# Kernel tuning notes

Hardware: AMD Instinct MI355X
Metric: run time of the kernel (lower is better)

The kernel has to match this reference:

```python
import jax, jax.numpy as jnp
import numpy as np

V, D, H, L, T_MAX = 50257, 1024, 16, 12, 256
HS = D // H
B, T = 8, 256


def setup_inputs() -> dict:
    key = jax.random.key(0)
    ks = jax.random.split(key, 24)
    s = 0.02
    inp = {
        'idx': jax.random.randint(ks[0], (B, T), 0, V),
        'targets': jax.random.randint(ks[1], (B, T), 0, V),
        'tok_emb': jax.random.normal(ks[2], (V, D), jnp.float32) * s,
        'pos_emb': jax.random.normal(ks[3], (T_MAX, D), jnp.float32) * s,
        'Wq': jax.random.normal(ks[4], (L, H, D, HS), jnp.float32) / np.sqrt(D),
        'Wk': jax.random.normal(ks[5], (L, H, D, HS), jnp.float32) / np.sqrt(D),
        'Wv': jax.random.normal(ks[6], (L, H, D, HS), jnp.float32) / np.sqrt(D),
        'ln1_g': jnp.ones((L, D), jnp.float32),
        'ln1_b': jnp.zeros((L, D), jnp.float32),
        'ln2_g': jnp.ones((L, D), jnp.float32),
        'ln2_b': jnp.zeros((L, D), jnp.float32),
        'fc1_w': jax.random.normal(ks[7], (L, D, 4 * D), jnp.float32) / np.sqrt(D),
        'fc1_b': jnp.zeros((L, 4 * D), jnp.float32),
        'fc2_w': jax.random.normal(ks[8], (L, 4 * D, D), jnp.float32) / np.sqrt(4 * D),
        'fc2_b': jnp.zeros((L, D), jnp.float32),
        'lnf_g': jnp.ones((D,), jnp.float32),
        'lnf_b': jnp.zeros((D,), jnp.float32),
        'lm_w': jax.random.normal(ks[9], (D, V), jnp.float32) / np.sqrt(D),
        'lm_b': jnp.zeros((V,), jnp.float32),
    }
    return inp


def _layernorm(x, g, b, eps=1e-5):
    mu = jnp.mean(x, axis=-1, keepdims=True)
    var = jnp.var(x, axis=-1, keepdims=True)
    return (x - mu) * jax.lax.rsqrt(var + eps) * g + b


def reference(idx, targets, tok_emb, pos_emb, Wq, Wk, Wv, ln1_g, ln1_b, ln2_g, ln2_b,
              fc1_w, fc1_b, fc2_w, fc2_b, lnf_g, lnf_b, lm_w, lm_b):
    Bc, Tc = idx.shape
    x = tok_emb[idx] + pos_emb[:Tc]  # [B,T,D]
    causal = jnp.tril(jnp.ones((Tc, Tc), bool))
    scale = 1.0 / np.sqrt(HS)
    for l in range(L):
        h = _layernorm(x, ln1_g[l], ln1_b[l])
        q = jnp.einsum('btd,hds->bhts', h, Wq[l])
        k = jnp.einsum('btd,hds->bhts', h, Wk[l])
        v = jnp.einsum('btd,hds->bhts', h, Wv[l])
        scores = jnp.einsum('bhts,bhus->bhtu', q, k) * scale
        scores = jnp.where(causal, scores, -jnp.inf)
        attn = jax.nn.softmax(scores, axis=-1)
        o = jnp.einsum('bhtu,bhus->bhts', attn, v)  # [B,H,T,hs]
        o = o.transpose(0, 2, 1, 3).reshape(Bc, Tc, D)  # concat heads
        x = x + o  # no output projection in original
        h = _layernorm(x, ln2_g[l], ln2_b[l])
        ff = jax.nn.relu(h @ fc1_w[l] + fc1_b[l]) @ fc2_w[l] + fc2_b[l]
        x = x + ff
    x = _layernorm(x, lnf_g, lnf_b)
    logits = x @ lm_w + lm_b  # [B,T,V]
    logp = jax.nn.log_softmax(logits, axis=-1)
    nll = -jnp.take_along_axis(logp, targets[..., None], axis=-1)[..., 0]
    loss = jnp.mean(nll)
    return logits, loss
```

## Files before the change

kernel.cpp:

```cpp
#include <hip/hip_runtime.h>

#define T_SEQ 256
#define DMODEL 1024
#define NHEAD 16
#define HSZ 64
#define NLAYER 12
#define VOCAB 50257
#define NPAD 50304
#define FF 4096
#define MROWS 2048

using short8 = __attribute__((ext_vector_type(8))) short;
using f32x4  = __attribute__((ext_vector_type(4))) float;

__device__ __forceinline__ float bf2f(unsigned short u) {
    unsigned int x = ((unsigned int)u) << 16;
    return __builtin_bit_cast(float, x);
}
__device__ __forceinline__ unsigned short f2bf(float f) {
    unsigned int u = __builtin_bit_cast(unsigned int, f);
    unsigned int r = (u + 0x7fffu + ((u >> 16) & 1u)) >> 16;
    return (unsigned short)r;
}
__device__ __forceinline__ void async_copy16(const void* g, void* l) {
    __builtin_amdgcn_global_load_lds(
        (const __attribute__((address_space(1))) unsigned int*)g,
        (__attribute__((address_space(3))) unsigned int*)l, 16, 0, 0);
}

__global__ __launch_bounds__(256) void embed_kernel(
    const int* __restrict__ idx, const float* __restrict__ tok,
    const float* __restrict__ pos, float* __restrict__ x)
{
    int row = blockIdx.x, tid = threadIdx.x;
    int t = row & (T_SEQ - 1);
    int token = idx[row];
    float4 a = ((const float4*)(tok + (size_t)token * DMODEL))[tid];
    float4 p = ((const float4*)(pos + (size_t)t * DMODEL))[tid];
    float4 o;
    o.x = a.x + p.x; o.y = a.y + p.y; o.z = a.z + p.z; o.w = a.w + p.w;
    ((float4*)(x + (size_t)row * DMODEL))[tid] = o;
}

__global__ __launch_bounds__(256) void ln_kernel(
    const float* __restrict__ x, const float* __restrict__ g,
    const float* __restrict__ b, unsigned short* __restrict__ out)
{
    int row = blockIdx.x, tid = threadIdx.x;
    float4 v = ((const float4*)(x + (size_t)row * DMODEL))[tid];
    float s  = v.x + v.y + v.z + v.w;
    float ss = v.x * v.x + v.y * v.y + v.z * v.z + v.w * v.w;
    for (int o = 32; o > 0; o >>= 1) {
        s  += __shfl_down(s, o);
        ss += __shfl_down(ss, o);
    }
    __shared__ float ps[4], pss[4];
    int wave = tid >> 6, lane = tid & 63;
    if (lane == 0) { ps[wave] = s; pss[wave] = ss; }
    __syncthreads();
    float st  = ps[0] + ps[1] + ps[2] + ps[3];
    float sst = pss[0] + pss[1] + pss[2] + pss[3];
    float mu  = st * (1.0f / DMODEL);
    float var = sst * (1.0f / DMODEL) - mu * mu;
    float rstd = rsqrtf(var + 1e-5f);
    float4 gv = ((const float4*)g)[tid];
    float4 bv = ((const float4*)b)[tid];
    ushort4 o4;
    o4.x = f2bf((v.x - mu) * rstd * gv.x + bv.x);
    o4.y = f2bf((v.y - mu) * rstd * gv.y + bv.y);
    o4.z = f2bf((v.z - mu) * rstd * gv.z + bv.z);
    o4.w = f2bf((v.w - mu) * rstd * gv.w + bv.w);
    ((ushort4*)out)[(size_t)row * (DMODEL / 4) + tid] = o4;
}

__global__ __launch_bounds__(256) void wtranspose_kernel(
    const float* __restrict__ in, unsigned short* __restrict__ out,
    int R, int C, int Cout, long in_l, long out_l)
{
    int lyr = blockIdx.z;
    in  += (size_t)lyr * in_l;
    out += (size_t)lyr * out_l;
    __shared__ float tile[32][33];
    int tx = threadIdx.x & 31, ty = threadIdx.x >> 5;
    int c0 = blockIdx.x * 32, r0 = blockIdx.y * 32;
    #pragma unroll
    for (int i = 0; i < 4; i++) {
        int r = r0 + ty + i * 8, c = c0 + tx;
        tile[ty + i * 8][tx] = (c < C) ? in[(size_t)r * C + c] : 0.f;
    }
    __syncthreads();
    #pragma unroll
    for (int i = 0; i < 4; i++) {
        int c = c0 + ty + i * 8, r = r0 + tx;
        if (c < Cout) out[(size_t)c * R + r] = f2bf(tile[tx][ty + i * 8]);
    }
}

__global__ __launch_bounds__(256) void qkvpack_kernel(
    const float* __restrict__ Wq, const float* __restrict__ Wk,
    const float* __restrict__ Wv, unsigned short* __restrict__ out,
    long w_l, long out_l)
{
    int z = blockIdx.z;
    int lyr = z / 48, r48 = z % 48;
    int seg = r48 >> 4, hh = r48 & 15;
    const float* W = (seg == 0 ? Wq : seg == 1 ? Wk : Wv)
                     + (size_t)lyr * w_l + (size_t)hh * DMODEL * HSZ;
    unsigned short* o = out + (size_t)lyr * out_l
                      + (size_t)(seg * 1024 + hh * 64) * DMODEL;
    __shared__ float tile[32][33];
    int tx = threadIdx.x & 31, ty = threadIdx.x >> 5;
    int d0 = blockIdx.x * 32, s0 = blockIdx.y * 32;
    #pragma unroll
    for (int i = 0; i < 4; i++)
        tile[ty + i * 8][tx] = W[(size_t)(d0 + ty + i * 8) * HSZ + s0 + tx];
    __syncthreads();
    #pragma unroll
    for (int i = 0; i < 4; i++)
        o[(size_t)(s0 + ty + i * 8) * DMODEL + d0 + tx] = f2bf(tile[tx][ty + i * 8]);
}

template<int MF, bool QKV, bool RELU, bool RES, bool CBF16>
__device__ __forceinline__ void gemm_core(
    const unsigned short* __restrict__ A, int lda,
    const unsigned short* __restrict__ Bt, int ldb,
    const float* __restrict__ bias,
    void* __restrict__ Cv, int ldc,
    const float* __restrict__ res, int ldr,
    int N, int K,
    unsigned short* __restrict__ vtout)
{
    constexpr int BM = MF * 32;
    __shared__ __align__(16) char As[BM * 128];
    __shared__ __align__(16) char Bs[128 * 128];
    int tid = threadIdx.x;
    int wave = tid >> 6, lane = tid & 63;
    int wr = wave >> 1, wc = wave & 1;
    int m0 = blockIdx.x * BM, n0 = blockIdx.y * 128;

    f32x4 acc[MF][4];
    #pragma unroll
    for (int m = 0; m < MF; m++)
        #pragma unroll
        for (int n = 0; n < 4; n++)
            acc[m][n] = (f32x4){0.f, 0.f, 0.f, 0.f};

    int ksw = (((lane & 7) ^ (lane >> 3)) << 4);
    int KT = K >> 6;
    for (int kt = 0; kt < KT; kt++) {
        int k0 = kt << 6;
        __syncthreads();
        #pragma unroll
        for (int j = 0; j < MF; j++) {
            int row = (wave * MF + j) * 8 + (lane >> 3);
            const char* src = (const char*)A + ((size_t)(m0 + row) * lda + k0) * 2 + ksw;
            async_copy16(src, As + (wave * MF + j) * 1024);
        }
        #pragma unroll
        for (int j = 0; j < 4; j++) {
            int nrow = (wave * 4 + j) * 8 + (lane >> 3);
            const char* src = (const char*)Bt + ((size_t)(n0 + nrow) * ldb + k0) * 2 + ksw;
            async_copy16(src, Bs + (wave * 4 + j) * 1024);
        }
        __syncthreads();
        #pragma unroll
        for (int ks = 0; ks < 2; ks++) {
            int kb = ks * 64 + ((lane >> 4) << 4);
            short8 a[MF], b[4];
            #pragma unroll
            for (int m = 0; m < MF; m++) {
                int r = wr * (MF * 16) + m * 16 + (lane & 15);
                a[m] = *(const short8*)(const void*)(As + r * 128 + (kb ^ ((r & 7) << 4)));
            }
            #pragma unroll
            for (int n = 0; n < 4; n++) {
                int c = wc * 64 + n * 16 + (lane & 15);
                b[n] = *(const short8*)(const void*)(Bs + c * 128 + (kb ^ ((c & 7) << 4)));
            }
            #pragma unroll
            for (int m = 0; m < MF; m++)
                #pragma unroll
                for (int n = 0; n < 4; n++)
                    acc[m][n] = __builtin_amdgcn_mfma_f32_16x16x32_bf16(a[m], b[n], acc[m][n], 0, 0, 0);
        }
    }
    #pragma unroll
    for (int m = 0; m < MF; m++) {
        int rowb = m0 + wr * (MF * 16) + m * 16 + ((lane >> 4) << 2);
        #pragma unroll
        for (int n = 0; n < 4; n++) {
            int col = n0 + wc * 64 + n * 16 + (lane & 15);
            if (col < N) {
                float bi = bias ? bias[col] : 0.f;
                #pragma unroll
                for (int r2 = 0; r2 < 4; r2++) {
                    float v = acc[m][n][r2] + bi;
                    if (RELU) v = fmaxf(v, 0.f);
                    int row = rowb + r2;
                    if (RES) v += res[(size_t)row * ldr + col];
                    if (QKV && col >= 2048) {
                        int hh = (col - 2048) >> 6, sdim = (col - 2048) & 63;
                        int bb = row >> 8, tt = row & 255;
                        vtout[((((size_t)bb * NHEAD + hh) * HSZ + sdim) * T_SEQ) + tt] = f2bf(v);
                    } else if (CBF16) {
                        ((unsigned short*)Cv)[(size_t)row * ldc + col] = f2bf(v);
                    } else {
                        ((float*)Cv)[(size_t)row * ldc + col] = v;
                    }
                }
            }
        }
    }
}

__global__ __launch_bounds__(256) void gemm_qkv(
    const unsigned short* __restrict__ A, const unsigned short* __restrict__ Bt,
    unsigned short* __restrict__ C, unsigned short* __restrict__ vtout)
{
    gemm_core<4, true, false, false, true>(
        A, DMODEL, Bt, DMODEL, nullptr, C, 3072, nullptr, 0, 3072, DMODEL, vtout);
}

__global__ __launch_bounds__(256) void gemm_fc1(
    const unsigned short* __restrict__ A, const unsigned short* __restrict__ Bt,
    const float* __restrict__ bias, unsigned short* __restrict__ C)
{
    gemm_core<4, false, true, false, true>(
        A, DMODEL, Bt, DMODEL, bias, C, FF, nullptr, 0, FF, DMODEL, nullptr);
}

__global__ __launch_bounds__(256) void gemm_fc2(
    const unsigned short* __restrict__ A, const unsigned short* __restrict__ Bt,
    float* __restrict__ part)
{
    int z = blockIdx.z;
    gemm_core<2, false, false, false, false>(
        A + z * 2048, FF, Bt + z * 2048, FF, nullptr,
        part + (size_t)z * MROWS * DMODEL, DMODEL, nullptr, 0,
        DMODEL, 2048, nullptr);
}

__global__ __launch_bounds__(256) void fc2_merge_kernel(
    const float* __restrict__ part, const float* __restrict__ bias,
    float* __restrict__ x)
{
    int row = blockIdx.x, tid = threadIdx.x;
    size_t o = (size_t)row * DMODEL / 4 + tid;
    float4 p0 = ((const float4*)part)[o];
    float4 p1 = ((const float4*)part)[o + MROWS * DMODEL / 4];
    float4 bv = ((const float4*)bias)[tid];
    float4 xv = ((float4*)x)[o];
    xv.x += p0.x + p1.x + bv.x;
    xv.y += p0.y + p1.y + bv.y;
    xv.z += p0.z + p1.z + bv.z;
    xv.w += p0.w + p1.w + bv.w;
    ((float4*)x)[o] = xv;
}

__global__ __launch_bounds__(256) void gemm_lm(
    const unsigned short* __restrict__ A, const unsigned short* __restrict__ Bt,
    const float* __restrict__ bias, float* __restrict__ C)
{
    gemm_core<4, false, false, false, false>(
        A, DMODEL, Bt, DMODEL, bias, C, VOCAB, nullptr, 0, VOCAB, DMODEL, nullptr);
}

__global__ __launch_bounds__(256) void attn_fused_kernel(
    const unsigned short* __restrict__ qkv, const unsigned short* __restrict__ vt,
    float* __restrict__ x)
{
    int qt = blockIdx.x, hh = blockIdx.y, b = blockIdx.z;
    int tid = threadIdx.x;
    int wave = tid >> 6, lane = tid & 63;
    int g = lane >> 4, q = lane & 15;

    __shared__ __align__(16) char Kb[2][8192];
    __shared__ __align__(16) char Vb[2][8192];
    __shared__ __align__(16) char Plds[4][2048];

    int qrow = b * T_SEQ + qt * 64 + wave * 16 + q;
    const char* qp = (const char*)qkv + ((size_t)qrow * 3072 + hh * HSZ) * 2;
    short8 qreg[2];
    qreg[0] = *(const short8*)(const void*)(qp + (g << 4));
    qreg[1] = *(const short8*)(const void*)(qp + 64 + (g << 4));

    char* Pw = Plds[wave];

    f32x4 oacc[4];
    #pragma unroll
    for (int f = 0; f < 4; f++) oacc[f] = (f32x4){0.f, 0.f, 0.f, 0.f};
    float m_run = -1e30f, l_run = 0.f;

    int srow = wave * 8 + (lane >> 3);
    int sbyte = ((lane & 7) << 4) ^ ((srow & 7) << 4);

    auto stage = [&](int kt, int bi) {
        #pragma unroll
        for (int c = 0; c < 2; c++) {
            int row = c * 32 + srow;
            const char* src = (const char*)qkv +
                ((size_t)(b * T_SEQ + kt * 64 + row) * 3072 + 1024 + hh * HSZ) * 2 + sbyte;
            async_copy16(src, Kb[bi] + c * 4096 + wave * 1024);
        }
        #pragma unroll
        for (int c = 0; c < 2; c++) {
            int row = c * 32 + srow;
            const char* src = (const char*)vt +
                (((size_t)(b * NHEAD + hh) * HSZ + row) * T_SEQ + kt * 64) * 2 + sbyte;
            async_copy16(src, Vb[bi] + c * 4096 + wave * 1024);
        }
    };

    stage(0, 0);
    for (int kt = 0; kt <= qt; kt++) {
        int bi = kt & 1;
        __syncthreads();
        if (kt < qt) stage(kt + 1, bi ^ 1);

        f32x4 sacc[4];
        #pragma unroll
        for (int f = 0; f < 4; f++) sacc[f] = (f32x4){0.f, 0.f, 0.f, 0.f};
        #pragma unroll
        for (int ks = 0; ks < 2; ks++) {
            int kb = ks * 64 + (g << 4);
            #pragma unroll
            for (int f = 0; f < 4; f++) {
                int u = f * 16 + q;
                short8 kf = *(const short8*)(const void*)(Kb[bi] + u * 128 + (kb ^ ((u & 7) << 4)));
                sacc[f] = __builtin_amdgcn_mfma_f32_16x16x32_bf16(kf, qreg[ks], sacc[f], 0, 0, 0);
            }
        }
        float sv[4][4];
        #pragma unroll
        for (int f = 0; f < 4; f++)
            #pragma unroll
            for (int r = 0; r < 4; r++) {
                float v = sacc[f][r] * 0.125f;
                if (kt == qt) {
                    int u_loc = f * 16 + g * 4 + r;
                    if (u_loc > wave * 16 + q) v = -1e30f;
                }
                sv[f][r] = v;
            }
        float pm = -1e30f;
        #pragma unroll
        for (int f = 0; f < 4; f++)
            #pragma unroll
            for (int r = 0; r < 4; r++) pm = fmaxf(pm, sv[f][r]);
        pm = fmaxf(pm, __shfl_xor(pm, 16));
        pm = fmaxf(pm, __shfl_xor(pm, 32));
        float mnew = fmaxf(m_run, pm);
        float corr = __expf(m_run - mnew);
        float p[4][4];
        float ls = 0.f;
        #pragma unroll
        for (int f = 0; f < 4; f++)
            #pragma unroll
            for (int r = 0; r < 4; r++) {
                p[f][r] = __expf(sv[f][r] - mnew);
                ls += p[f][r];
            }
        ls += __shfl_xor(ls, 16);
        ls += __shfl_xor(ls, 32);
        l_run = l_run * corr + ls;
        m_run = mnew;
        #pragma unroll
        for (int r = 0; r < 4; r++) {
            float cr = __shfl(corr, (lane & 48) | (g * 4 + r));
            #pragma unroll
            for (int f = 0; f < 4; f++) oacc[f][r] *= cr;
        }
        #pragma unroll
        for (int f = 0; f < 4; f++)
            #pragma unroll
            for (int rp = 0; rp < 2; rp++) {
                int ue = f * 16 + g * 4 + rp * 2;
                unsigned int pk = (unsigned int)f2bf(p[f][rp * 2])
                                | ((unsigned int)f2bf(p[f][rp * 2 + 1]) << 16);
                *(unsigned int*)(void*)(Pw + q * 128 + ((ue * 2) ^ ((q & 7) << 4))) = pk;
            }
        #pragma unroll
        for (int ks = 0; ks < 2; ks++) {
            int kb = ks * 64 + (g << 4);
            short8 pa = *(const short8*)(const void*)(Pw + q * 128 + (kb ^ ((q & 7) << 4)));
            #pragma unroll
            for (int f = 0; f < 4; f++) {
                int s = f * 16 + q;
                short8 vf = *(const short8*)(const void*)(Vb[bi] + s * 128 + (kb ^ ((s & 7) << 4)));
                oacc[f] = __builtin_amdgcn_mfma_f32_16x16x32_bf16(pa, vf, oacc[f], 0, 0, 0);
            }
        }
    }
    float inv = 1.0f / l_run;
    #pragma unroll
    for (int r = 0; r < 4; r++) {
        float ir = __shfl(inv, (lane & 48) | (g * 4 + r));
        int row_g = b * T_SEQ + qt * 64 + wave * 16 + g * 4 + r;
        #pragma unroll
        for (int f = 0; f < 4; f++) {
            size_t xi = (size_t)row_g * DMODEL + hh * HSZ + f * 16 + q;
            x[xi] += oacc[f][r] * ir;
        }
    }
}

__global__ __launch_bounds__(256) void loss1_kernel(
    const float* __restrict__ logits, const int* __restrict__ targets,
    float* __restrict__ nll)
{
    int r = blockIdx.x, tid = threadIdx.x;
    const float* row = logits + (size_t)r * VOCAB;
    const float4* row4 = (const float4*)row;
    float m = -3.4e38f, s = 0.f;
    for (int v = tid; v < VOCAB / 4; v += 256) {
        float4 x4 = row4[v];
        float lm = fmaxf(fmaxf(x4.x, x4.y), fmaxf(x4.z, x4.w));
        float nm = fmaxf(m, lm);
        s = s * __expf(m - nm) + __expf(x4.x - nm) + __expf(x4.y - nm)
          + __expf(x4.z - nm) + __expf(x4.w - nm);
        m = nm;
    }
    if (tid == 0) {
        float xv = row[VOCAB - 1];
        float nm = fmaxf(m, xv);
        s = s * __expf(m - nm) + __expf(xv - nm);
        m = nm;
    }
    __shared__ float ms[256], ssh[256];
    ms[tid] = m; ssh[tid] = s;
    __syncthreads();
    for (int o = 128; o > 0; o >>= 1) {
        if (tid < o) {
            float m1 = ms[tid], s1 = ssh[tid];
            float m2 = ms[tid + o], s2 = ssh[tid + o];
            float nm = fmaxf(m1, m2);
            ssh[tid] = s1 * __expf(m1 - nm) + s2 * __expf(m2 - nm);
            ms[tid] = nm;
        }
        __syncthreads();
    }
    if (tid == 0) nll[r] = logf(ssh[0]) + ms[0] - row[targets[r]];
}

__global__ __launch_bounds__(256) void loss2_kernel(
    const float* __restrict__ nll, float* __restrict__ out)
{
    int tid = threadIdx.x;
    float s = 0.f;
    for (int i = tid; i < MROWS; i += 256) s += nll[i];
    __shared__ float red[256];
    red[tid] = s;
    __syncthreads();
    for (int o = 128; o > 0; o >>= 1) {
        if (tid < o) red[tid] += red[tid + o];
        __syncthreads();
    }
    if (tid == 0) out[0] = red[0] * (1.0f / MROWS);
}

extern "C" void kernel_launch(void* const* d_in, const int* in_sizes, int n_in,
                              void* d_out, int out_size, void* d_ws, size_t ws_size,
                              hipStream_t stream)
{
    const int*   idx  = (const int*)d_in[0];
    const int*   tgt  = (const int*)d_in[1];
    const float* tok  = (const float*)d_in[2];
    const float* pos  = (const float*)d_in[3];
    const float* Wq   = (const float*)d_in[4];
    const float* Wk   = (const float*)d_in[5];
    const float* Wv   = (const float*)d_in[6];
    const float* ln1g = (const float*)d_in[7];
    const float* ln1b = (const float*)d_in[8];
    const float* ln2g = (const float*)d_in[9];
    const float* ln2b = (const float*)d_in[10];
    const float* fc1w = (const float*)d_in[11];
    const float* fc1b = (const float*)d_in[12];
    const float* fc2w = (const float*)d_in[13];
    const float* fc2b = (const float*)d_in[14];
    const float* lnfg = (const float*)d_in[15];
    const float* lnfb = (const float*)d_in[16];
    const float* lmw  = (const float*)d_in[17];
    const float* lmb  = (const float*)d_in[18];

    char* ws = (char*)d_ws;
    float*          x    = (float*)(ws + 0);
    unsigned short* h    = (unsigned short*)(ws + 8388608);
    unsigned short* qkv  = (unsigned short*)(ws + 12582912);
    unsigned short* vt   = (unsigned short*)(ws + 25165824);
    unsigned short* mid  = (unsigned short*)(ws + 29360128);
    float*          nll  = (float*)(ws + 46137344);
    float*          fc2p = (float*)(ws + 46145536);
    unsigned short* lmwt = (unsigned short*)(ws + 62922752);
    const size_t UP_NEED = 442769408ull;
    bool upfront = (ws_size >= UP_NEED);
    unsigned short* qkvt = (unsigned short*)(ws + 165945344);
    unsigned short* fc1t, * fc2t;
    long qkvt_l, fc1t_l, fc2t_l;
    if (upfront) {
        fc1t = (unsigned short*)(ws + 241442816);
        fc2t = (unsigned short*)(ws + 342106112);
        qkvt_l = 3072 * 1024; fc1t_l = (long)FF * 1024; fc2t_l = (long)1024 * FF;
    } else {
        fc1t = (unsigned short*)(ws + 172236800);
        fc2t = (unsigned short*)(ws + 180625408);
        qkvt_l = 0; fc1t_l = 0; fc2t_l = 0;
    }
    float* logits = (float*)d_out;
    float* lossp  = logits + (size_t)MROWS * VOCAB;

    const long WQKV_L = (long)NHEAD * DMODEL * HSZ;
    if (upfront) {
        qkvpack_kernel<<<dim3(32, 2, 48 * NLAYER), 256, 0, stream>>>(
            Wq, Wk, Wv, qkvt, WQKV_L, qkvt_l);
        wtranspose_kernel<<<dim3(128, 32, NLAYER), 256, 0, stream>>>(
            fc1w, fc1t, DMODEL, FF, FF, (long)DMODEL * FF, fc1t_l);
        wtranspose_kernel<<<dim3(32, 128, NLAYER), 256, 0, stream>>>(
            fc2w, fc2t, FF, DMODEL, DMODEL, (long)FF * DMODEL, fc2t_l);
    }
    wtranspose_kernel<<<dim3(1572, 32, 1), 256, 0, stream>>>(
        lmw, lmwt, DMODEL, VOCAB, NPAD, 0, 0);

    embed_kernel<<<MROWS, 256, 0, stream>>>(idx, tok, pos, x);

    for (int l = 0; l < NLAYER; l++) {
        unsigned short* qkvt_p = qkvt + (size_t)l * qkvt_l;
        unsigned short* fc1t_p = fc1t + (size_t)l * fc1t_l;
        unsigned short* fc2t_p = fc2t + (size_t)l * fc2t_l;
        if (!upfront) {
            qkvpack_kernel<<<dim3(32, 2, 48), 256, 0, stream>>>(
                Wq + (size_t)l * WQKV_L, Wk + (size_t)l * WQKV_L,
                Wv + (size_t)l * WQKV_L, qkvt, WQKV_L, 0);
            wtranspose_kernel<<<dim3(128, 32, 1), 256, 0, stream>>>(
                fc1w + (size_t)l * DMODEL * FF, fc1t, DMODEL, FF, FF, 0, 0);
            wtranspose_kernel<<<dim3(32, 128, 1), 256, 0, stream>>>(
                fc2w + (size_t)l * FF * DMODEL, fc2t, FF, DMODEL, DMODEL, 0, 0);
        }
        ln_kernel<<<MROWS, 256, 0, stream>>>(x, ln1g + l * DMODEL, ln1b + l * DMODEL, h);
        gemm_qkv<<<dim3(16, 24), 256, 0, stream>>>(h, qkvt_p, qkv, vt);
        attn_fused_kernel<<<dim3(4, NHEAD, 8), 256, 0, stream>>>(qkv, vt, x);
        ln_kernel<<<MROWS, 256, 0, stream>>>(x, ln2g + l * DMODEL, ln2b + l * DMODEL, h);
        gemm_fc1<<<dim3(16, 32), 256, 0, stream>>>(h, fc1t_p, fc1b + (size_t)l * FF, mid);
        gemm_fc2<<<dim3(32, 8, 2), 256, 0, stream>>>(mid, fc2t_p, fc2p);
        fc2_merge_kernel<<<MROWS, 256, 0, stream>>>(fc2p, fc2b + (size_t)l * DMODEL, x);
    }

    ln_kernel<<<MROWS, 256, 0, stream>>>(x, lnfg, lnfb, h);
    gemm_lm<<<dim3(16, 393), 256, 0, stream>>>(h, lmwt, lmb, logits);

    loss1_kernel<<<MROWS, 256, 0, stream>>>(logits, tgt, nll);
    loss2_kernel<<<1, 256, 0, stream>>>(nll, lossp);
}
```

Baseline: 2.223 ms.

## Double-buffer GEMM LDS tiles and fuse layernorm into embed and fc2 merge

The shared GEMM core now keeps two LDS buffers and issues the async global-to-LDS loads for the next K tile before computing on the current one, so only one barrier per iteration remains. LDS use per block doubles, which may lower occupancy. The embedding and fc2-merge kernels now also compute the following layernorm (ln1 of the next layer or the final one), removing 13 separate layernorm launches and their re-read of the residual stream.

```diff
diff --git a/kernel.cpp b/kernel.cpp
--- a/kernel.cpp
+++ b/kernel.cpp
@@ -28,26 +28,10 @@
         (__attribute__((address_space(3))) unsigned int*)l, 16, 0, 0);
 }
 
-__global__ __launch_bounds__(256) void embed_kernel(
-    const int* __restrict__ idx, const float* __restrict__ tok,
-    const float* __restrict__ pos, float* __restrict__ x)
-{
-    int row = blockIdx.x, tid = threadIdx.x;
-    int t = row & (T_SEQ - 1);
-    int token = idx[row];
-    float4 a = ((const float4*)(tok + (size_t)token * DMODEL))[tid];
-    float4 p = ((const float4*)(pos + (size_t)t * DMODEL))[tid];
-    float4 o;
-    o.x = a.x + p.x; o.y = a.y + p.y; o.z = a.z + p.z; o.w = a.w + p.w;
-    ((float4*)(x + (size_t)row * DMODEL))[tid] = o;
-}
-
-__global__ __launch_bounds__(256) void ln_kernel(
-    const float* __restrict__ x, const float* __restrict__ g,
-    const float* __restrict__ b, unsigned short* __restrict__ out)
-{
-    int row = blockIdx.x, tid = threadIdx.x;
-    float4 v = ((const float4*)(x + (size_t)row * DMODEL))[tid];
+__device__ __forceinline__ void ln_tail(
+    float4 v, const float* __restrict__ g, const float* __restrict__ b,
+    int row, int tid, unsigned short* __restrict__ out)
+{
     float s  = v.x + v.y + v.z + v.w;
     float ss = v.x * v.x + v.y * v.y + v.z * v.z + v.w * v.w;
     for (int o = 32; o > 0; o >>= 1) {
@@ -73,6 +57,51 @@
     ((ushort4*)out)[(size_t)row * (DMODEL / 4) + tid] = o4;
 }
 
+__global__ __launch_bounds__(256) void embed_ln_kernel(
+    const int* __restrict__ idx, const float* __restrict__ tok,
+    const float* __restrict__ pos, const float* __restrict__ g,
+    const float* __restrict__ b, float* __restrict__ x,
+    unsigned short* __restrict__ h)
+{
+    int row = blockIdx.x, tid = threadIdx.x;
+    int t = row & (T_SEQ - 1);
+    int token = idx[row];
+    float4 a = ((const float4*)(tok + (size_t)token * DMODEL))[tid];
+    float4 p = ((const float4*)(pos + (size_t)t * DMODEL))[tid];
+    float4 v;
+    v.x = a.x + p.x; v.y = a.y + p.y; v.z = a.z + p.z; v.w = a.w + p.w;
+    ((float4*)(x + (size_t)row * DMODEL))[tid] = v;
+    ln_tail(v, g, b, row, tid, h);
+}
+
+__global__ __launch_bounds__(256) void ln_kernel(
+    const float* __restrict__ x, const float* __restrict__ g,
+    const float* __restrict__ b, unsigned short* __restrict__ out)
+{
+    int row = blockIdx.x, tid = threadIdx.x;
+    float4 v = ((const float4*)(x + (size_t)row * DMODEL))[tid];
+    ln_tail(v, g, b, row, tid, out);
+}
+
+__global__ __launch_bounds__(256) void fc2_merge_ln_kernel(
+    const float* __restrict__ part, const float* __restrict__ bias,
+    const float* __restrict__ g, const float* __restrict__ b,
+    float* __restrict__ x, unsigned short* __restrict__ h)
+{
+    int row = blockIdx.x, tid = threadIdx.x;
+    size_t o = (size_t)row * (DMODEL / 4) + tid;
+    float4 p0 = ((const float4*)part)[o];
+    float4 p1 = ((const float4*)part)[o + MROWS * (DMODEL / 4)];
+    float4 bv = ((const float4*)bias)[tid];
+    float4 v = ((float4*)x)[o];
+    v.x += p0.x + p1.x + bv.x;
+    v.y += p0.y + p1.y + bv.y;
+    v.z += p0.z + p1.z + bv.z;
+    v.w += p0.w + p1.w + bv.w;
+    ((float4*)x)[o] = v;
+    ln_tail(v, g, b, row, tid, h);
+}
+
 __global__ __launch_bounds__(256) void wtranspose_kernel(
     const float* __restrict__ in, unsigned short* __restrict__ out,
     int R, int C, int Cout, long in_l, long out_l)
@@ -131,8 +160,8 @@
     unsigned short* __restrict__ vtout)
 {
     constexpr int BM = MF * 32;
-    __shared__ __align__(16) char As[BM * 128];
-    __shared__ __align__(16) char Bs[128 * 128];
+    __shared__ __align__(16) char As[2][BM * 128];
+    __shared__ __align__(16) char Bs[2][128 * 128];
     int tid = threadIdx.x;
     int wave = tid >> 6, lane = tid & 63;
     int wr = wave >> 1, wc = wave & 1;
@@ -147,22 +176,28 @@
 
     int ksw = (((lane & 7) ^ (lane >> 3)) << 4);
     int KT = K >> 6;
-    for (int kt = 0; kt < KT; kt++) {
+
+    auto stage = [&](int kt, int bi) {
         int k0 = kt << 6;
-        __syncthreads();
         #pragma unroll
         for (int j = 0; j < MF; j++) {
             int row = (wave * MF + j) * 8 + (lane >> 3);
             const char* src = (const char*)A + ((size_t)(m0 + row) * lda + k0) * 2 + ksw;
-            async_copy16(src, As + (wave * MF + j) * 1024);
+            async_copy16(src, As[bi] + (wave * MF + j) * 1024);
         }
         #pragma unroll
         for (int j = 0; j < 4; j++) {
             int nrow = (wave * 4 + j) * 8 + (lane >> 3);
             const char* src = (const char*)Bt + ((size_t)(n0 + nrow) * ldb + k0) * 2 + ksw;
-            async_copy16(src, Bs + (wave * 4 + j) * 1024);
-        }
-        __syncthreads();
+            async_copy16(src, Bs[bi] + (wave * 4 + j) * 1024);
+        }
+    };
+
+    stage(0, 0);
+    __syncthreads();
+    int cur = 0;
+    for (int kt = 0; kt < KT; kt++) {
+        if (kt + 1 < KT) stage(kt + 1, cur ^ 1);
         #pragma unroll
         for (int ks = 0; ks < 2; ks++) {
             int kb = ks * 64 + ((lane >> 4) << 4);
@@ -170,12 +205,12 @@
             #pragma unroll
             for (int m = 0; m < MF; m++) {
                 int r = wr * (MF * 16) + m * 16 + (lane & 15);
-                a[m] = *(const short8*)(const void*)(As + r * 128 + (kb ^ ((r & 7) << 4)));
+                a[m] = *(const short8*)(const void*)(As[cur] + r * 128 + (kb ^ ((r & 7) << 4)));
             }
             #pragma unroll
             for (int n = 0; n < 4; n++) {
                 int c = wc * 64 + n * 16 + (lane & 15);
-                b[n] = *(const short8*)(const void*)(Bs + c * 128 + (kb ^ ((c & 7) << 4)));
+                b[n] = *(const short8*)(const void*)(Bs[cur] + c * 128 + (kb ^ ((c & 7) << 4)));
             }
             #pragma unroll
             for (int m = 0; m < MF; m++)
@@ -183,6 +218,8 @@
                 for (int n = 0; n < 4; n++)
                     acc[m][n] = __builtin_amdgcn_mfma_f32_16x16x32_bf16(a[m], b[n], acc[m][n], 0, 0, 0);
         }
+        __syncthreads();
+        cur ^= 1;
     }
     #pragma unroll
     for (int m = 0; m < MF; m++) {
@@ -238,23 +275,6 @@
         A + z * 2048, FF, Bt + z * 2048, FF, nullptr,
         part + (size_t)z * MROWS * DMODEL, DMODEL, nullptr, 0,
         DMODEL, 2048, nullptr);
-}
-
-__global__ __launch_bounds__(256) void fc2_merge_kernel(
-    const float* __restrict__ part, const float* __restrict__ bias,
-    float* __restrict__ x)
-{
-    int row = blockIdx.x, tid = threadIdx.x;
-    size_t o = (size_t)row * DMODEL / 4 + tid;
-    float4 p0 = ((const float4*)part)[o];
-    float4 p1 = ((const float4*)part)[o + MROWS * DMODEL / 4];
-    float4 bv = ((const float4*)bias)[tid];
-    float4 xv = ((float4*)x)[o];
-    xv.x += p0.x + p1.x + bv.x;
-    xv.y += p0.y + p1.y + bv.y;
-    xv.z += p0.z + p1.z + bv.z;
-    xv.w += p0.w + p1.w + bv.w;
-    ((float4*)x)[o] = xv;
 }
 
 __global__ __launch_bounds__(256) void gemm_lm(
@@ -520,7 +540,7 @@
     wtranspose_kernel<<<dim3(1572, 32, 1), 256, 0, stream>>>(
         lmw, lmwt, DMODEL, VOCAB, NPAD, 0, 0);
 
-    embed_kernel<<<MROWS, 256, 0, stream>>>(idx, tok, pos, x);
+    embed_ln_kernel<<<MROWS, 256, 0, stream>>>(idx, tok, pos, ln1g, ln1b, x, h);
 
     for (int l = 0; l < NLAYER; l++) {
         unsigned short* qkvt_p = qkvt + (size_t)l * qkvt_l;
@@ -535,16 +555,17 @@
             wtranspose_kernel<<<dim3(32, 128, 1), 256, 0, stream>>>(
                 fc2w + (size_t)l * FF * DMODEL, fc2t, FF, DMODEL, DMODEL, 0, 0);
         }
-        ln_kernel<<<MROWS, 256, 0, stream>>>(x, ln1g + l * DMODEL, ln1b + l * DMODEL, h);
         gemm_qkv<<<dim3(16, 24), 256, 0, stream>>>(h, qkvt_p, qkv, vt);
         attn_fused_kernel<<<dim3(4, NHEAD, 8), 256, 0, stream>>>(qkv, vt, x);
         ln_kernel<<<MROWS, 256, 0, stream>>>(x, ln2g + l * DMODEL, ln2b + l * DMODEL, h);
         gemm_fc1<<<dim3(16, 32), 256, 0, stream>>>(h, fc1t_p, fc1b + (size_t)l * FF, mid);
         gemm_fc2<<<dim3(32, 8, 2), 256, 0, stream>>>(mid, fc2t_p, fc2p);
-        fc2_merge_kernel<<<MROWS, 256, 0, stream>>>(fc2p, fc2b + (size_t)l * DMODEL, x);
-    }
-
-    ln_kernel<<<MROWS, 256, 0, stream>>>(x, lnfg, lnfb, h);
+        const float* ng = (l < NLAYER - 1) ? ln1g + (l + 1) * DMODEL : lnfg;
+        const float* nb = (l < NLAYER - 1) ? ln1b + (l + 1) * DMODEL : lnfb;
+        fc2_merge_ln_kernel<<<MROWS, 256, 0, stream>>>(
+            fc2p, fc2b + (size_t)l * DMODEL, ng, nb, x, h);
+    }
+
     gemm_lm<<<dim3(16, 393), 256, 0, stream>>>(h, lmwt, lmb, logits);
 
     loss1_kernel<<<MROWS, 256, 0, stream>>>(logits, tgt, nll);
```

After: 2.257 ms. Within noise of the previous version (+1.5%).
